# Kernel optimization log

Measured on AMD Instinct MI355X. Metric: run time of the kernel, lower is better.

The kernel has to match this reference:

```python
import jax, jax.numpy as jnp
import numpy as np

WS = 16                     # window_size
OW = 24                     # overlap_win_size = int(16*0.5)+16
PAD = (OW - WS) // 2        # unfold padding = 4
DIM = 384
HEADS = 6
HID = 768                   # mlp_ratio 2.0 * dim
TABLE = (WS + OW - 1) ** 2  # 1521


def _rel_pos_index():
    ch = np.arange(WS)
    coords = np.stack(np.meshgrid(ch, ch, indexing='ij')).reshape(2, -1)      # (2, WS*WS)
    co = np.arange(OW)
    coords_o = np.stack(np.meshgrid(co, co, indexing='ij')).reshape(2, -1)    # (2, OW*OW)
    rel = coords[:, :, None] - coords_o[:, None, :]                           # (2, nq, nk)
    rel = rel.transpose(1, 2, 0).astype(np.int64)
    rel[..., 0] += OW - 1
    rel[..., 1] += OW - 1
    rel[..., 0] *= WS + OW - 1
    return rel.sum(-1)                                                        # (WS*WS, OW*OW)

RPI = jnp.asarray(_rel_pos_index())


def _ln(x, g, b, eps=1e-5):
    m = x.mean(-1, keepdims=True)
    v = ((x - m) ** 2).mean(-1, keepdims=True)
    return (x - m) / jnp.sqrt(v + eps) * g + b


def _overlap_windows(t, H, W):
    # t: (B,H,W,C) -> (B*nw, OW*OW, C); overlapping patches, stride WS, pad PAD
    B, _, _, C = t.shape
    nH, nW = H // WS, W // WS
    tp = jnp.pad(t, ((0, 0), (PAD, PAD), (PAD, PAD), (0, 0)))
    r = (jnp.arange(nH) * WS)[:, None] + jnp.arange(OW)   # (nH, OW)
    c = (jnp.arange(nW) * WS)[:, None] + jnp.arange(OW)   # (nW, OW)
    p = tp[:, r]              # (B, nH, OW, Wp, C)
    p = p[:, :, :, c]         # (B, nH, OW, nW, OW, C)
    p = p.transpose(0, 1, 3, 2, 4, 5).reshape(B * nH * nW, OW * OW, C)
    return p


def setup_inputs() -> dict:
    key = jax.random.key(0)
    ks = jax.random.split(key, 8)
    H = W = 192
    B = 1
    inp = {
        'x': jax.random.normal(ks[0], (B, H * W, DIM), dtype=jnp.float32),
        'norm1_g': jnp.ones((DIM,), jnp.float32),
        'norm1_b': jnp.zeros((DIM,), jnp.float32),
        'qkv_w': jax.random.normal(ks[1], (DIM, 3 * DIM), jnp.float32) * 0.02,
        'qkv_b': jnp.zeros((3 * DIM,), jnp.float32),
        'rpb_table': jax.random.normal(ks[2], (TABLE, HEADS), jnp.float32) * 0.02,
        'proj_w': jax.random.normal(ks[3], (DIM, DIM), jnp.float32) * 0.02,
        'proj_b': jnp.zeros((DIM,), jnp.float32),
        'norm2_g': jnp.ones((DIM,), jnp.float32),
        'norm2_b': jnp.zeros((DIM,), jnp.float32),
        'fc1_w': jax.random.normal(ks[4], (DIM, HID), jnp.float32) * 0.02,
        'fc1_b': jnp.zeros((HID,), jnp.float32),
        'fc2_w': jax.random.normal(ks[5], (HID, DIM), jnp.float32) * 0.02,
        'fc2_b': jnp.zeros((DIM,), jnp.float32),
        'H': H,
        'W': W,
    }
    return inp


def reference(x, norm1_g, norm1_b, qkv_w, qkv_b, rpb_table, proj_w, proj_b,
              norm2_g, norm2_b, fc1_w, fc1_b, fc2_w, fc2_b, H, W):
    B, L, C = x.shape
    d = C // HEADS
    scale = d ** (-0.5)
    nH, nW = H // WS, W // WS

    shortcut = x
    xn = _ln(x, norm1_g, norm1_b).reshape(B, H, W, C)
    qkv = xn @ qkv_w + qkv_b                                   # (B,H,W,3C)
    q, k, v = qkv[..., :C], qkv[..., C:2 * C], qkv[..., 2 * C:]

    # non-overlapping query windows: (B*nw, WS*WS, C)
    qw = q.reshape(B, nH, WS, nW, WS, C).transpose(0, 1, 3, 2, 4, 5).reshape(-1, WS * WS, C)
    # overlapping key/value windows: (B*nw, OW*OW, C)
    kw = _overlap_windows(k, H, W)
    vw = _overlap_windows(v, H, W)

    b_ = qw.shape[0]
    qh = qw.reshape(b_, WS * WS, HEADS, d) * scale
    kh = kw.reshape(b_, OW * OW, HEADS, d)
    vh = vw.reshape(b_, OW * OW, HEADS, d)

    attn = jnp.einsum('bqhd,bkhd->bhqk', qh, kh)               # (b_, H, nq, nk)
    bias = rpb_table[RPI].transpose(2, 0, 1)                   # (heads, nq, nk)
    attn = jax.nn.softmax(attn + bias[None], axis=-1)
    out = jnp.einsum('bhqk,bkhd->bqhd', attn, vh).reshape(b_, WS * WS, C)

    # window reverse -> (B, H*W, C)
    out = out.reshape(B, nH, nW, WS, WS, C).transpose(0, 1, 3, 2, 4, 5).reshape(B, H * W, C)
    out = out @ proj_w + proj_b

    x = shortcut + out
    h = _ln(x, norm2_g, norm2_b)
    h = jax.nn.gelu(h @ fc1_w + fc1_b, approximate=False)
    h = h @ fc2_w + fc2_b
    return x + h
```

## Files before the change

### kernel.cpp

```cpp
#include <hip/hip_runtime.h>

#define LTOK 36864
#define DIMC 384
#define NHEADS 6
#define HDIM 64
#define HIDD 768
#define NWIN 12
#define WSZ 16
#define OWS 24
#define KVTOK 576

using bf16x8 = __attribute__((ext_vector_type(8))) short;
using f32x4  = __attribute__((ext_vector_type(4))) float;

__device__ inline unsigned short f2bf(float f) {
  unsigned u = __float_as_uint(f);
  return (unsigned short)((u + 0x7FFFu + ((u >> 16) & 1u)) >> 16);
}
__device__ __forceinline__ unsigned cvt_pk_bf16(float lo, float hi) {
  unsigned r;
  asm volatile("v_cvt_pk_bf16_f32 %0, %1, %2" : "=v"(r) : "v"(lo), "v"(hi));
  return r;
}
__device__ __forceinline__ unsigned short f2bf1(float x) {
  return (unsigned short)(cvt_pk_bf16(x, x) & 0xffffu);
}
__device__ __forceinline__ float fexp2(float x) {
#if __has_builtin(__builtin_amdgcn_exp2f)
  return __builtin_amdgcn_exp2f(x);
#else
  return exp2f(x);
#endif
}

typedef __attribute__((address_space(1))) const unsigned int GAS_U32;
typedef __attribute__((address_space(3))) unsigned int LAS_U32;
__device__ __forceinline__ void gl16(const void* g, void* l) {
  __builtin_amdgcn_global_load_lds((GAS_U32*)g, (LAS_U32*)l, 16, 0, 0);
}

__global__ void prep_kernel(const float* __restrict__ qkv_w, const float* __restrict__ proj_w,
                            const float* __restrict__ fc1_w, const float* __restrict__ fc2_w,
                            unsigned short* __restrict__ wq, unsigned short* __restrict__ wp,
                            unsigned short* __restrict__ w1, unsigned short* __restrict__ w2) {
  int id = blockIdx.x * 256 + threadIdx.x;
  if (id < 442368) {
    int n = id / 384, k = id - n * 384;
    wq[id] = f2bf(qkv_w[(size_t)k * 1152 + n]);
  } else if (id < 589824) {
    int i = id - 442368;
    int n = i / 384, k = i - n * 384;
    wp[i] = f2bf(proj_w[(size_t)k * 384 + n]);
  } else if (id < 884736) {
    int i = id - 589824;
    int n = i / 384, k = i - n * 384;
    w1[i] = f2bf(fc1_w[(size_t)k * 768 + n]);
  } else {
    int i = id - 884736;
    int n = i / 768, k = i - n * 768;
    w2[i] = f2bf(fc2_w[(size_t)k * 384 + n]);
  }
}

__global__ void rpb_expand_kernel(const float* __restrict__ rpb, float* __restrict__ biasm8) {
  int id = blockIdx.x * 256 + threadIdx.x;
  if (id >= NHEADS * 256 * 576) return;
  int head = id / 147456;
  int rem = id - head * 147456;
  int q = rem / 576;
  int kt = rem - q * 576;
  int ty = q >> 4, tx = q & 15;
  int oy = kt / 24, ox = kt - (kt / 24) * 24;
  biasm8[id] = rpb[((ty - oy + 23) * 39 + (tx - ox + 23)) * NHEADS + head] * 8.0f;
}

__global__ __launch_bounds__(256) void ln_kernel(const float* __restrict__ x,
                                                 const float* __restrict__ g,
                                                 const float* __restrict__ b,
                                                 unsigned short* __restrict__ out) {
  int row = blockIdx.x * 4 + (threadIdx.x >> 6);
  int lane = threadIdx.x & 63;
  const float* xr = x + (size_t)row * DIMC;
  float v[6];
  float s = 0.f, ss = 0.f;
#pragma unroll
  for (int i = 0; i < 6; ++i) {
    v[i] = xr[lane + i * 64];
    s += v[i];
    ss += v[i] * v[i];
  }
#pragma unroll
  for (int off = 32; off; off >>= 1) {
    s += __shfl_xor(s, off);
    ss += __shfl_xor(ss, off);
  }
  float mean = s * (1.f / DIMC);
  float var = ss * (1.f / DIMC) - mean * mean;
  float rstd = rsqrtf(var + 1e-5f);
  unsigned short* outr = out + (size_t)row * DIMC;
#pragma unroll
  for (int i = 0; i < 6; ++i) {
    int c = lane + i * 64;
    outr[c] = f2bf((v[i] - mean) * rstd * g[c] + b[c]);
  }
}

template <int EPI>
__global__ __launch_bounds__(256) void gemm_bf16(const unsigned short* __restrict__ A,
                                                 const unsigned short* __restrict__ Bt,
                                                 const float* __restrict__ bias,
                                                 const float* __restrict__ resid,
                                                 void* __restrict__ outv,
                                                 int M, int N, int K) {
  __shared__ unsigned short As[2][8192];
  __shared__ unsigned short Bs[2][8192];
  const int tid = threadIdx.x;
  int id = blockIdx.y * gridDim.x + blockIdx.x;
  int chunk = (gridDim.x * gridDim.y) >> 3;
  int lid = (id & 7) * chunk + (id >> 3);
  const int m0 = (lid / gridDim.x) * 128;
  const int n0 = (lid % gridDim.x) * 128;
  const int lane = tid & 63;
  const int wave = tid >> 6;
  const int wr = wave >> 1;
  const int wc = wave & 1;
  const int l15 = lane & 15, l4 = lane >> 4;

  f32x4 acc[4][4];
#pragma unroll
  for (int i = 0; i < 4; ++i)
#pragma unroll
    for (int j = 0; j < 4; ++j) acc[i][j] = (f32x4){0.f, 0.f, 0.f, 0.f};

  const int srow = wave * 8 + (lane >> 3);
  const int scol = (lane & 7) << 3;
  const unsigned short* ga = A + (size_t)(m0 + srow) * K + scol;
  const unsigned short* gb = Bt + (size_t)(n0 + srow) * K + scol;

#define STAGE(buf, k0)                                                     \
  do {                                                                     \
    _Pragma("unroll") for (int p = 0; p < 4; ++p) {                        \
      gl16(ga + (size_t)(p * 32) * K + (k0), As[buf] + p * 2048 + wave * 512); \
      gl16(gb + (size_t)(p * 32) * K + (k0), Bs[buf] + p * 2048 + wave * 512); \
    }                                                                      \
  } while (0)

  STAGE(0, 0);
  __syncthreads();

  const int nt = K >> 6;
  for (int t = 0; t < nt; ++t) {
    const int cur = t & 1;
    if (t + 1 < nt) STAGE(cur ^ 1, (t + 1) * 64);

#pragma unroll
    for (int kk = 0; kk < 2; ++kk) {
      const char* ab = (const char*)As[cur] + (wr * 64 + l15) * 128 + kk * 64 + l4 * 16;
      const char* bb = (const char*)Bs[cur] + (wc * 64 + l15) * 128 + kk * 64 + l4 * 16;
      bf16x8 af[4], bfr[4];
#pragma unroll
      for (int i = 0; i < 4; ++i) af[i] = *(const bf16x8*)(ab + i * 2048);
#pragma unroll
      for (int j = 0; j < 4; ++j) bfr[j] = *(const bf16x8*)(bb + j * 2048);
#pragma unroll
      for (int i = 0; i < 4; ++i)
#pragma unroll
        for (int j = 0; j < 4; ++j)
          acc[i][j] = __builtin_amdgcn_mfma_f32_16x16x32_bf16(af[i], bfr[j], acc[i][j], 0, 0, 0);
    }

    __syncthreads();
  }
#undef STAGE

#pragma unroll
  for (int j = 0; j < 4; ++j) {
    int gcol = n0 + wc * 64 + j * 16 + l15;
    float bv = bias[gcol];
#pragma unroll
    for (int i = 0; i < 4; ++i) {
#pragma unroll
      for (int r = 0; r < 4; ++r) {
        int grow = m0 + wr * 64 + i * 16 + l4 * 4 + r;
        float v = acc[i][j][r] + bv;
        size_t idx = (size_t)grow * N + gcol;
        if (EPI == 0) {
          ((unsigned short*)outv)[idx] = f2bf(v);
        } else if (EPI == 1) {
          ((float*)outv)[idx] = resid[idx] + v;
        } else {
          float gv = 0.5f * v * (1.f + erff(v * 0.70710678118654752f));
          ((unsigned short*)outv)[idx] = f2bf(gv);
        }
      }
    }
  }
}

__global__ __launch_bounds__(256, 3) void attn_kernel(const unsigned short* __restrict__ qkv,
                                                      const float* __restrict__ biasm8,
                                                      unsigned short* __restrict__ att) {
  __shared__ unsigned short ks[2][64][72];
  __shared__ unsigned short vts[2][64][72];
  __shared__ unsigned short pt[4][32][40];
  int bid = blockIdx.x;
  int lid = (bid & 7) * 216 + (bid >> 3);
  const int hw = lid >> 1;
  const int qh = lid & 1;
  const int win = hw / NHEADS;
  const int head = hw - win * NHEADS;
  const int wy = win / NWIN, wx = win - (win / NWIN) * NWIN;
  const int tid = threadIdx.x;
  const int w = tid >> 6, lane = tid & 63;
  const int l15 = lane & 15, l4 = lane >> 4;
  const float SC02 = 0.125f * 1.44269504f;
  const float C0 = -8.f * 1.44269504f;

  const int qrow0 = qh * 128 + w * 32;

  bf16x8 qf[2][2];
#pragma unroll
  for (int jq = 0; jq < 2; ++jq) {
    int q = qrow0 + jq * 16 + l15;
    int gy = wy * WSZ + (q >> 4), gx = wx * WSZ + (q & 15);
    const unsigned short* qp = qkv + (size_t)(gy * 192 + gx) * 1152 + head * HDIM + l4 * 8;
    qf[jq][0] = *(const bf16x8*)qp;
    qf[jq][1] = *(const bf16x8*)(qp + 32);
  }

  const float* bias_base = biasm8 + (size_t)head * 147456 + (size_t)(qrow0 + l15) * 576 + l4 * 4;

#define KS_W(buf, k0v, k1v)                          \
  do {                                               \
    *(uint4*)&ks[buf][lane][w * 16] = (k0v);         \
    *(uint4*)&ks[buf][lane][w * 16 + 8] = (k1v);     \
  } while (0)
#define VTS_W(buf, v0v, v1v)                                           \
  do {                                                                 \
    const unsigned short* vv = (const unsigned short*)&(v0v);          \
    _Pragma("unroll") for (int j = 0; j < 8; ++j)                      \
        vts[buf][w * 16 + j][lane] = vv[j];                            \
    vv = (const unsigned short*)&(v1v);                                \
    _Pragma("unroll") for (int j = 0; j < 8; ++j)                      \
        vts[buf][w * 16 + 8 + j][lane] = vv[j];                        \
  } while (0)

  {
    int kt = lane;
    int oy = kt / OWS, ox = kt - (kt / OWS) * OWS;
    int gy = wy * WSZ + oy - 4, gx = wx * WSZ + ox - 4;
    uint4 k0 = {0,0,0,0}, k1 = {0,0,0,0}, v0 = {0,0,0,0}, v1 = {0,0,0,0};
    if ((unsigned)gy < 192u && (unsigned)gx < 192u) {
      const unsigned short* gp = qkv + (size_t)(gy * 192 + gx) * 1152 + DIMC + head * HDIM + w * 16;
      k0 = *(const uint4*)gp;         k1 = *(const uint4*)(gp + 8);
      v0 = *(const uint4*)(gp + 384); v1 = *(const uint4*)(gp + 392);
    }
    KS_W(0, k0, k1);
    VTS_W(0, v0, v1);
  }

  f32x4 sacc[4][2];
#pragma unroll
  for (int i = 0; i < 4; ++i)
#pragma unroll
    for (int j2 = 0; j2 < 2; ++j2)
      sacc[i][j2] = *(const f32x4*)(bias_base + j2 * (16 * 576) + i * 16);

  __syncthreads();

  f32x4 oacc[2][4];
#pragma unroll
  for (int i = 0; i < 2; ++i)
#pragma unroll
    for (int j = 0; j < 4; ++j) oacc[i][j] = (f32x4){0.f, 0.f, 0.f, 0.f};
  float plsum[2] = {0.f, 0.f};

  for (int kb = 0; kb < 9; ++kb) {
    const int cur = kb & 1;
    const bool have = kb < 8;
    uint4 pk0 = {0,0,0,0}, pk1 = {0,0,0,0}, pv0 = {0,0,0,0}, pv1 = {0,0,0,0};
    if (have) {
      int kt = (kb + 1) * 64 + lane;
      int oy = kt / OWS, ox = kt - (kt / OWS) * OWS;
      int gy = wy * WSZ + oy - 4, gx = wx * WSZ + ox - 4;
      if ((unsigned)gy < 192u && (unsigned)gx < 192u) {
        const unsigned short* gp = qkv + (size_t)(gy * 192 + gx) * 1152 + DIMC + head * HDIM + w * 16;
        pk0 = *(const uint4*)gp;         pk1 = *(const uint4*)(gp + 8);
        pv0 = *(const uint4*)(gp + 384); pv1 = *(const uint4*)(gp + 392);
      }
    }

#pragma unroll
    for (int kk = 0; kk < 2; ++kk) {
      bf16x8 kf[4];
#pragma unroll
      for (int i = 0; i < 4; ++i)
        kf[i] = *(const bf16x8*)&ks[cur][i * 16 + l15][kk * 32 + l4 * 8];
      __builtin_amdgcn_s_setprio(1);
#pragma unroll
      for (int i = 0; i < 4; ++i)
#pragma unroll
        for (int j2 = 0; j2 < 2; ++j2)
          sacc[i][j2] = __builtin_amdgcn_mfma_f32_16x16x32_bf16(kf[i], qf[j2][kk], sacc[i][j2], 0, 0, 0);
      __builtin_amdgcn_s_setprio(0);
    }

#pragma unroll
    for (int i = 0; i < 4; ++i)
#pragma unroll
      for (int j2 = 0; j2 < 2; ++j2)
#pragma unroll
        for (int r = 0; r < 4; ++r) {
          float p = fexp2(fmaf(sacc[i][j2][r], SC02, C0));
          sacc[i][j2][r] = p;
          plsum[j2] += p;
        }

#pragma unroll
    for (int kk = 0; kk < 2; ++kk) {
#pragma unroll
      for (int i2 = 0; i2 < 2; ++i2)
#pragma unroll
        for (int j2 = 0; j2 < 2; ++j2) {
          int i = kk * 2 + i2;
          uint2 pk;
          pk.x = cvt_pk_bf16(sacc[i][j2][0], sacc[i][j2][1]);
          pk.y = cvt_pk_bf16(sacc[i][j2][2], sacc[i][j2][3]);
          *(uint2*)&pt[w][j2 * 16 + l15][i2 * 16 + l4 * 4] = pk;
        }
      bf16x8 pf[2], vf[4];
#pragma unroll
      for (int j2 = 0; j2 < 2; ++j2)
        pf[j2] = *(const bf16x8*)&pt[w][j2 * 16 + l15][l4 * 8];
#pragma unroll
      for (int jd = 0; jd < 4; ++jd)
        vf[jd] = *(const bf16x8*)&vts[cur][jd * 16 + l15][kk * 32 + l4 * 8];
      __builtin_amdgcn_s_setprio(1);
#pragma unroll
      for (int j2 = 0; j2 < 2; ++j2)
#pragma unroll
        for (int jd = 0; jd < 4; ++jd)
          oacc[j2][jd] = __builtin_amdgcn_mfma_f32_16x16x32_bf16(pf[j2], vf[jd], oacc[j2][jd], 0, 0, 0);
      __builtin_amdgcn_s_setprio(0);
    }

    if (have) {
      KS_W(cur ^ 1, pk0, pk1);
      VTS_W(cur ^ 1, pv0, pv1);
      const float* bp = bias_base + (kb + 1) * 64;
#pragma unroll
      for (int i = 0; i < 4; ++i)
#pragma unroll
        for (int j2 = 0; j2 < 2; ++j2)
          sacc[i][j2] = *(const f32x4*)(bp + j2 * (16 * 576) + i * 16);
    }
    __syncthreads();
  }
#undef KS_W
#undef VTS_W

  float invl[2];
#pragma unroll
  for (int j2 = 0; j2 < 2; ++j2) {
    plsum[j2] += __shfl_xor(plsum[j2], 16);
    plsum[j2] += __shfl_xor(plsum[j2], 32);
    invl[j2] = 1.f / plsum[j2];
  }

#pragma unroll
  for (int j2 = 0; j2 < 2; ++j2) {
#pragma unroll
    for (int r = 0; r < 4; ++r) {
      float il = __shfl(invl[j2], l4 * 4 + r);
      int q = qrow0 + j2 * 16 + l4 * 4 + r;
      int gy = wy * WSZ + (q >> 4), gx = wx * WSZ + (q & 15);
      unsigned short* op = att + (size_t)(gy * 192 + gx) * DIMC + head * HDIM + l15;
#pragma unroll
      for (int jd = 0; jd < 4; ++jd) op[jd * 16] = f2bf1(oacc[j2][jd][r] * il);
    }
  }
}

extern "C" void kernel_launch(void* const* d_in, const int* in_sizes, int n_in,
                              void* d_out, int out_size, void* d_ws, size_t ws_size,
                              hipStream_t stream) {
  const float* x      = (const float*)d_in[0];
  const float* n1g    = (const float*)d_in[1];
  const float* n1b    = (const float*)d_in[2];
  const float* qkv_w  = (const float*)d_in[3];
  const float* qkv_b  = (const float*)d_in[4];
  const float* rpb    = (const float*)d_in[5];
  const float* proj_w = (const float*)d_in[6];
  const float* proj_b = (const float*)d_in[7];
  const float* n2g    = (const float*)d_in[8];
  const float* n2b    = (const float*)d_in[9];
  const float* fc1_w  = (const float*)d_in[10];
  const float* fc1_b  = (const float*)d_in[11];
  const float* fc2_w  = (const float*)d_in[12];
  const float* fc2_b  = (const float*)d_in[13];
  float* out = (float*)d_out;

  char* ws = (char*)d_ws;
  unsigned short* xn   = (unsigned short*)ws;
  unsigned short* qkvb = (unsigned short*)(ws + 28311552);
  unsigned short* att  = (unsigned short*)(ws + 28311552 + 84934656);
  unsigned short* wq   = (unsigned short*)(ws + 141557760);
  unsigned short* wp   = wq + 1152 * 384;
  unsigned short* w1   = wp + 384 * 384;
  unsigned short* w2   = w1 + 768 * 384;
  float* biasm8 = (float*)ws;

  prep_kernel<<<4608, 256, 0, stream>>>(qkv_w, proj_w, fc1_w, fc2_w, wq, wp, w1, w2);

  ln_kernel<<<LTOK / 4, 256, 0, stream>>>(x, n1g, n1b, xn);
  gemm_bf16<0><<<dim3(1152 / 128, LTOK / 128), 256, 0, stream>>>(xn, wq, qkv_b, nullptr, qkvb,
                                                                 LTOK, 1152, DIMC);
  rpb_expand_kernel<<<(NHEADS * 256 * 576 + 255) / 256, 256, 0, stream>>>(rpb, biasm8);
  attn_kernel<<<dim3(NHEADS * 144 * 2), 256, 0, stream>>>(qkvb, biasm8, att);
  gemm_bf16<1><<<dim3(DIMC / 128, LTOK / 128), 256, 0, stream>>>(att, wp, proj_b, x, out,
                                                                 LTOK, DIMC, DIMC);
  ln_kernel<<<LTOK / 4, 256, 0, stream>>>(out, n2g, n2b, xn);
  gemm_bf16<2><<<dim3(HIDD / 128, LTOK / 128), 256, 0, stream>>>(xn, w1, fc1_b, nullptr, qkvb,
                                                                 LTOK, HIDD, DIMC);
  gemm_bf16<1><<<dim3(DIMC / 128, LTOK / 128), 256, 0, stream>>>(qkvb, w2, fc2_b, out, out,
                                                                 LTOK, DIMC, HIDD);
}
```

Before: 344.2 us.

## Triple-buffer GEMM LDS stages with BK=32 and vmcnt-based prefetch depth two

```diff
diff --git a/kernel.cpp b/kernel.cpp
--- a/kernel.cpp
+++ b/kernel.cpp
@@ -112,8 +112,8 @@
                                                  const float* __restrict__ resid,
                                                  void* __restrict__ outv,
                                                  int M, int N, int K) {
-  __shared__ unsigned short As[2][8192];
-  __shared__ unsigned short Bs[2][8192];
+  __shared__ unsigned short As[3][4096];
+  __shared__ unsigned short Bs[3][4096];
   const int tid = threadIdx.x;
   int id = blockIdx.y * gridDim.x + blockIdx.x;
   int chunk = (gridDim.x * gridDim.y) >> 3;
@@ -132,46 +132,47 @@
 #pragma unroll
     for (int j = 0; j < 4; ++j) acc[i][j] = (f32x4){0.f, 0.f, 0.f, 0.f};
 
-  const int srow = wave * 8 + (lane >> 3);
-  const int scol = (lane & 7) << 3;
+  const int srow = tid >> 2;
+  const int scol = (tid & 3) << 3;
   const unsigned short* ga = A + (size_t)(m0 + srow) * K + scol;
   const unsigned short* gb = Bt + (size_t)(n0 + srow) * K + scol;
 
-#define STAGE(buf, k0)                                                     \
-  do {                                                                     \
-    _Pragma("unroll") for (int p = 0; p < 4; ++p) {                        \
-      gl16(ga + (size_t)(p * 32) * K + (k0), As[buf] + p * 2048 + wave * 512); \
-      gl16(gb + (size_t)(p * 32) * K + (k0), Bs[buf] + p * 2048 + wave * 512); \
-    }                                                                      \
+#define STAGE(buf, k0)                                        \
+  do {                                                        \
+    unsigned short* lA = As[buf] + wave * 512;                \
+    unsigned short* lB = Bs[buf] + wave * 512;                \
+    gl16(ga + (k0), lA);                                      \
+    gl16(ga + (size_t)64 * K + (k0), lA + 2048);              \
+    gl16(gb + (k0), lB);                                      \
+    gl16(gb + (size_t)64 * K + (k0), lB + 2048);              \
   } while (0)
 
+  const int nt = K >> 5;
   STAGE(0, 0);
-  __syncthreads();
-
-  const int nt = K >> 6;
+  STAGE(1, 32);
+
   for (int t = 0; t < nt; ++t) {
-    const int cur = t & 1;
-    if (t + 1 < nt) STAGE(cur ^ 1, (t + 1) * 64);
-
-#pragma unroll
-    for (int kk = 0; kk < 2; ++kk) {
-      const char* ab = (const char*)As[cur] + (wr * 64 + l15) * 128 + kk * 64 + l4 * 16;
-      const char* bb = (const char*)Bs[cur] + (wc * 64 + l15) * 128 + kk * 64 + l4 * 16;
-      bf16x8 af[4], bfr[4];
-#pragma unroll
-      for (int i = 0; i < 4; ++i) af[i] = *(const bf16x8*)(ab + i * 2048);
-#pragma unroll
-      for (int j = 0; j < 4; ++j) bfr[j] = *(const bf16x8*)(bb + j * 2048);
-#pragma unroll
-      for (int i = 0; i < 4; ++i)
-#pragma unroll
-        for (int j = 0; j < 4; ++j)
-          acc[i][j] = __builtin_amdgcn_mfma_f32_16x16x32_bf16(af[i], bfr[j], acc[i][j], 0, 0, 0);
-    }
-
-    __syncthreads();
+    const int cur = t % 3;
+    asm volatile("s_waitcnt vmcnt(4)" ::: "memory");
+    __builtin_amdgcn_s_barrier();
+
+    if (t + 2 < nt) STAGE((t + 2) % 3, (t + 2) * 32);
+
+    const unsigned short* arp = As[cur] + (wr * 64 + l15) * 32 + l4 * 8;
+    const unsigned short* brp = Bs[cur] + (wc * 64 + l15) * 32 + l4 * 8;
+    bf16x8 af[4], bfr[4];
+#pragma unroll
+    for (int i = 0; i < 4; ++i) af[i] = *(const bf16x8*)(arp + i * 512);
+#pragma unroll
+    for (int j = 0; j < 4; ++j) bfr[j] = *(const bf16x8*)(brp + j * 512);
+#pragma unroll
+    for (int i = 0; i < 4; ++i)
+#pragma unroll
+      for (int j = 0; j < 4; ++j)
+        acc[i][j] = __builtin_amdgcn_mfma_f32_16x16x32_bf16(af[i], bfr[j], acc[i][j], 0, 0, 0);
   }
 #undef STAGE
+  asm volatile("s_waitcnt vmcnt(0)" ::: "memory");
 
 #pragma unroll
   for (int j = 0; j < 4; ++j) {
```

Result: faster. 330.9 us (-3.8%).
